# Performance work log

Hardware: AMD Instinct MI355X
Metric: run time of the kernel (lower is better)

The kernel has to match this reference:

```python
import jax, jax.numpy as jnp
import numpy as np

NUM_IN, NUM_OUT, SD, BATCH = 2048, 8192, 5, 4096
INIT_DELTA = 0.01


def _dist(a, b):
    # a: [I,1,D], b: [1,O,D] -> [I,O]
    return jnp.sqrt(jnp.sum((a - b) ** 2, axis=-1))


def setup_inputs() -> dict:
    key = jax.random.key(0)
    k1, k2, k3, k4, k5 = jax.random.split(key, 5)
    init_in_pos = jax.random.normal(k1, (NUM_IN, 1, SD), dtype=jnp.float32)
    init_out_pos = jax.random.normal(k2, (1, NUM_OUT, SD), dtype=jnp.float32)
    in_pos = init_in_pos + INIT_DELTA * jax.random.normal(k3, (NUM_IN, 1, SD), dtype=jnp.float32)
    out_pos = init_out_pos + INIT_DELTA * jax.random.normal(k4, (1, NUM_OUT, SD), dtype=jnp.float32)
    inputs = jax.random.normal(k5, (BATCH, NUM_IN), dtype=jnp.float32)
    biases = jnp.zeros((NUM_OUT,), dtype=jnp.float32)
    return {"inputs": inputs, "init_in_pos": init_in_pos, "init_out_pos": init_out_pos,
            "in_pos": in_pos, "out_pos": out_pos, "biases": biases}


def reference(inputs, init_in_pos, init_out_pos, in_pos, out_pos, biases):
    # weight = ||in_pos - out_pos|| - ||init_in_pos - init_out_pos||, shape [I,O]
    w = _dist(in_pos, out_pos) - _dist(init_in_pos, init_out_pos)
    return inputs @ w + biases
```

## Files before the change

kernel.cpp:

```cpp
#include <hip/hip_runtime.h>
#include <hip/hip_bf16.h>
#include <stdint.h>

#define NUM_IN  2048
#define NUM_OUT 8192
#define BATCH   4096
#define SD      5

#define BM 256
#define BN 256
#define BK 64
#define NT (NUM_IN / BK)
#define NI (NT / 2)
#define TILEE (BM * BK)

typedef __bf16 bf16x8 __attribute__((ext_vector_type(8)));
typedef float  f32x4  __attribute__((ext_vector_type(4)));
typedef unsigned short ushort_t;
typedef ushort_t ushort8 __attribute__((ext_vector_type(8)));

static __device__ __forceinline__ ushort_t bf16_bits(float f) {
  __hip_bfloat16 h = __float2bfloat16(f);
  ushort_t u;
  __builtin_memcpy(&u, &h, 2);
  return u;
}

__global__ __launch_bounds__(256) void cvt_kernel(const float* __restrict__ x,
                                                  ushort_t* __restrict__ y) {
  const int i = (blockIdx.x * 256 + threadIdx.x) * 8;
  float4 v0 = *reinterpret_cast<const float4*>(x + i);
  float4 v1 = *reinterpret_cast<const float4*>(x + i + 4);
  ushort8 o;
  o[0] = bf16_bits(v0.x); o[1] = bf16_bits(v0.y);
  o[2] = bf16_bits(v0.z); o[3] = bf16_bits(v0.w);
  o[4] = bf16_bits(v1.x); o[5] = bf16_bits(v1.y);
  o[6] = bf16_bits(v1.z); o[7] = bf16_bits(v1.w);
  *reinterpret_cast<ushort8*>(y + i) = o;
}

__global__ __launch_bounds__(256) void genw_kernel(
    const float* __restrict__ in_pos, const float* __restrict__ out_pos,
    const float* __restrict__ init_in, const float* __restrict__ init_out,
    ushort_t* __restrict__ Wt) {
  __shared__ float s_ip[NUM_IN * SD];
  __shared__ float s_iip[NUM_IN * SD];
  const int tid = threadIdx.x;
#pragma unroll
  for (int i = 0; i < 10; ++i) {
    const int idx = i * 1024 + tid * 4;
    *reinterpret_cast<float4*>(&s_ip[idx]) =
        *reinterpret_cast<const float4*>(in_pos + idx);
    *reinterpret_cast<float4*>(&s_iip[idx]) =
        *reinterpret_cast<const float4*>(init_in + idx);
  }
  __syncthreads();

  const int n  = blockIdx.x * 16 + (tid >> 4);
  const int kg = tid & 15;
  float op[SD], iop[SD];
#pragma unroll
  for (int d = 0; d < SD; ++d) {
    op[d]  = out_pos[n * SD + d];
    iop[d] = init_out[n * SD + d];
  }
#pragma unroll 1
  for (int kb = 0; kb < 16; ++kb) {
    const int k0 = kb * 128 + kg * 8;
    float buf[40], ibuf[40];
#pragma unroll
    for (int j = 0; j < 10; ++j) {
      float4 v = *reinterpret_cast<const float4*>(&s_ip[k0 * SD + j * 4]);
      buf[4 * j + 0] = v.x; buf[4 * j + 1] = v.y;
      buf[4 * j + 2] = v.z; buf[4 * j + 3] = v.w;
      float4 u = *reinterpret_cast<const float4*>(&s_iip[k0 * SD + j * 4]);
      ibuf[4 * j + 0] = u.x; ibuf[4 * j + 1] = u.y;
      ibuf[4 * j + 2] = u.z; ibuf[4 * j + 3] = u.w;
    }
    ushort8 o;
#pragma unroll
    for (int i = 0; i < 8; ++i) {
      float d1 = 0.f, d0 = 0.f;
#pragma unroll
      for (int d = 0; d < SD; ++d) {
        float a = buf[i * SD + d] - op[d];
        float b = ibuf[i * SD + d] - iop[d];
        d1 += a * a;
        d0 += b * b;
      }
      o[i] = bf16_bits(sqrtf(d1) - sqrtf(d0));
    }
    *reinterpret_cast<ushort8*>(Wt + (size_t)n * NUM_IN + k0) = o;
  }
}

__global__ __launch_bounds__(512, 1) void gemm_kernel(
    const ushort_t* __restrict__ A,
    const ushort_t* __restrict__ Bt,
    const float* __restrict__ bias,
    float* __restrict__ C) {
  __shared__ __align__(16) ushort_t sA[2 * TILEE];
  __shared__ __align__(16) ushort_t sB[2 * TILEE];

  const int tid  = threadIdx.x;
  const int w    = tid >> 6;
  const int l    = tid & 63;
  const int wm   = w >> 2;
  const int wn   = w & 3;
  const int lrow = l & 15;
  const int lkc  = l >> 4;

  const int orig = blockIdx.x;
  const int lin  = (orig & 7) * 64 + (orig >> 3);
  const int bx   = lin >> 4;
  const int by   = lin & 15;
  const int m0   = by * BM;
  const int n0   = bx * BN;

  const int ck0 = (lkc ^ (lrow & 7)) * 8;
  const int ck1 = ((4 + lkc) ^ (lrow & 7)) * 8;
  const int Ab  = wm * 4096 + lrow * 64;
  const int Bb  = wn * 2048 + lrow * 64;

  const int d0 = tid, d1 = tid + 512;
  const int lr0 = d0 >> 3, lr1 = d1 >> 3;
  const int c0 = (d0 & 7) ^ (lr0 & 7);
  const int c1 = (d1 & 7) ^ (lr1 & 7);
  const ushort_t* pA0 = A  + (size_t)(m0 + (lr0 >> 6) * 128 + (lr0 & 63)) * NUM_IN + c0 * 8;
  const ushort_t* pA1 = A  + (size_t)(m0 + (lr1 >> 6) * 128 + (lr1 & 63)) * NUM_IN + c1 * 8;
  const ushort_t* pB0 = Bt + (size_t)(n0 + (lr0 >> 5) * 64 + (lr0 & 31)) * NUM_IN + c0 * 8;
  const ushort_t* pB1 = Bt + (size_t)(n0 + (lr1 >> 5) * 64 + (lr1 & 31)) * NUM_IN + c1 * 8;

#define GLDS(src, dst)                                                         \
  __builtin_amdgcn_global_load_lds(                                            \
      reinterpret_cast<const __attribute__((address_space(1))) uint32_t*>(     \
          (uintptr_t)(src)),                                                   \
      reinterpret_cast<__attribute__((address_space(3))) uint32_t*>(           \
          (uintptr_t)(dst)),                                                   \
      16, 0, 0)

#define STAGE_A(bs, mh, kt)                                                    \
  {                                                                            \
    GLDS(pA0 + (size_t)(mh) * 64 * NUM_IN + (kt),                              \
         &sA[(bs) * TILEE + (mh) * 8192 + tid * 8]);                           \
    GLDS(pA1 + (size_t)(mh) * 64 * NUM_IN + (kt),                              \
         &sA[(bs) * TILEE + (mh) * 8192 + tid * 8 + 4096]);                    \
  }
#define STAGE_B(bs, nh, kt)                                                    \
  {                                                                            \
    GLDS(pB0 + (size_t)(nh) * 32 * NUM_IN + (kt),                              \
         &sB[(bs) * TILEE + (nh) * 8192 + tid * 8]);                           \
    GLDS(pB1 + (size_t)(nh) * 32 * NUM_IN + (kt),                              \
         &sB[(bs) * TILEE + (nh) * 8192 + tid * 8 + 4096]);                    \
  }

#define RD_A(bs, mh)                                                           \
  {                                                                            \
    _Pragma("unroll")                                                          \
    for (int mi = 0; mi < 4; ++mi) {                                           \
      a[mi][0] = *reinterpret_cast<const bf16x8*>(                             \
          &sA[(bs) * TILEE + (mh) * 8192 + Ab + mi * 1024 + ck0]);             \
      a[mi][1] = *reinterpret_cast<const bf16x8*>(                             \
          &sA[(bs) * TILEE + (mh) * 8192 + Ab + mi * 1024 + ck1]);             \
    }                                                                          \
  }
#define RD_B(bs, nh, arr)                                                      \
  {                                                                            \
    _Pragma("unroll")                                                          \
    for (int nj = 0; nj < 2; ++nj) {                                           \
      arr[nj][0] = *reinterpret_cast<const bf16x8*>(                           \
          &sB[(bs) * TILEE + (nh) * 8192 + Bb + nj * 1024 + ck0]);             \
      arr[nj][1] = *reinterpret_cast<const bf16x8*>(                           \
          &sB[(bs) * TILEE + (nh) * 8192 + Bb + nj * 1024 + ck1]);             \
    }                                                                          \
  }

#define MFMA_Q(mh, nh, arr)                                                    \
  {                                                                            \
    __builtin_amdgcn_s_setprio(1);                                             \
    _Pragma("unroll")                                                          \
    for (int mi = 0; mi < 4; ++mi)                                             \
      _Pragma("unroll")                                                        \
      for (int nj = 0; nj < 2; ++nj) {                                         \
        acc[(mh) * 4 + mi][(nh) * 2 + nj] =                                    \
            __builtin_amdgcn_mfma_f32_16x16x32_bf16(                           \
                a[mi][0], arr[nj][0], acc[(mh) * 4 + mi][(nh) * 2 + nj],       \
                0, 0, 0);                                                      \
        acc[(mh) * 4 + mi][(nh) * 2 + nj] =                                    \
            __builtin_amdgcn_mfma_f32_16x16x32_bf16(                           \
                a[mi][1], arr[nj][1], acc[(mh) * 4 + mi][(nh) * 2 + nj],       \
                0, 0, 0);                                                      \
      }                                                                        \
    __builtin_amdgcn_s_setprio(0);                                             \
  }

#define BARRIER  __builtin_amdgcn_s_barrier()
#define SCHED0   __builtin_amdgcn_sched_barrier(0)
#define LGKM0    asm volatile("s_waitcnt lgkmcnt(0)" ::: "memory")
#define VMCNT4   asm volatile("s_waitcnt vmcnt(4)" ::: "memory")

  f32x4 acc[8][4];
#pragma unroll
  for (int i = 0; i < 8; ++i)
#pragma unroll
    for (int j = 0; j < 4; ++j) acc[i][j] = f32x4{0.f, 0.f, 0.f, 0.f};

  STAGE_A(0, 0, 0) STAGE_B(0, 0, 0) STAGE_A(0, 1, 0) STAGE_B(0, 1, 0)
  STAGE_A(1, 0, BK) STAGE_B(1, 0, BK)
  VMCNT4;
  BARRIER;
  SCHED0;

#pragma unroll 1
  for (int it = 0; it < NI; ++it) {
    const int t1k = (2 * it + 1) * BK;
    const int t2  = 2 * it + 2, t3 = 2 * it + 3;
    const int t2k = (t2 < NT ? t2 : NT - 1) * BK;
    const int t3k = (t3 < NT ? t3 : NT - 1) * BK;
    bf16x8 a[4][2], b0[2][2], b1[2][2];

    RD_A(0, 0) RD_B(0, 0, b0)
    STAGE_A(1, 1, t1k)
    BARRIER; LGKM0; SCHED0;
    MFMA_Q(0, 0, b0)
    BARRIER; SCHED0;

    RD_B(0, 1, b1)
    STAGE_B(1, 1, t1k)
    BARRIER; LGKM0; SCHED0;
    MFMA_Q(0, 1, b1)
    BARRIER; SCHED0;

    RD_A(0, 1)
    STAGE_A(0, 0, t2k)
    BARRIER; LGKM0; SCHED0;
    MFMA_Q(1, 0, b0)
    BARRIER; SCHED0;

    STAGE_B(0, 0, t2k)
    BARRIER; SCHED0;
    MFMA_Q(1, 1, b1)
    VMCNT4;
    BARRIER; SCHED0;

    RD_A(1, 0) RD_B(1, 0, b0)
    STAGE_A(0, 1, t2k)
    BARRIER; LGKM0; SCHED0;
    MFMA_Q(0, 0, b0)
    BARRIER; SCHED0;

    RD_B(1, 1, b1)
    STAGE_B(0, 1, t2k)
    BARRIER; LGKM0; SCHED0;
    MFMA_Q(0, 1, b1)
    BARRIER; SCHED0;

    RD_A(1, 1)
    STAGE_A(1, 0, t3k)
    BARRIER; LGKM0; SCHED0;
    MFMA_Q(1, 0, b0)
    BARRIER; SCHED0;

    STAGE_B(1, 0, t3k)
    BARRIER; SCHED0;
    MFMA_Q(1, 1, b1)
    VMCNT4;
    BARRIER; SCHED0;
  }

  const int er = l >> 4;
  const int ec = l & 15;
#pragma unroll
  for (int nh = 0; nh < 2; ++nh) {
#pragma unroll
    for (int nj = 0; nj < 2; ++nj) {
      const int col = n0 + wn * 64 + nh * 32 + nj * 16 + ec;
      const float bi = bias[col];
#pragma unroll
      for (int mh = 0; mh < 2; ++mh) {
#pragma unroll
        for (int mi = 0; mi < 4; ++mi) {
#pragma unroll
          for (int j = 0; j < 4; ++j) {
            const int row = m0 + wm * 128 + mh * 64 + mi * 16 + er * 4 + j;
            C[(size_t)row * NUM_OUT + col] =
                acc[mh * 4 + mi][nh * 2 + nj][j] + bi;
          }
        }
      }
    }
  }
#undef STAGE_A
#undef STAGE_B
#undef RD_A
#undef RD_B
#undef MFMA_Q
#undef GLDS
}

extern "C" void kernel_launch(void* const* d_in, const int* in_sizes, int n_in,
                              void* d_out, int out_size, void* d_ws, size_t ws_size,
                              hipStream_t stream) {
  const float* inputs   = (const float*)d_in[0];
  const float* init_in  = (const float*)d_in[1];
  const float* init_out = (const float*)d_in[2];
  const float* in_pos   = (const float*)d_in[3];
  const float* out_pos  = (const float*)d_in[4];
  const float* biases   = (const float*)d_in[5];
  float* out = (float*)d_out;

  ushort_t* Abf = (ushort_t*)d_ws;
  ushort_t* Wt  = (ushort_t*)((char*)d_ws + (size_t)BATCH * NUM_IN * 2);

  cvt_kernel<<<(BATCH * NUM_IN) / (256 * 8), 256, 0, stream>>>(inputs, Abf);
  genw_kernel<<<NUM_OUT / 16, 256, 0, stream>>>(
      in_pos, out_pos, init_in, init_out, Wt);
  gemm_kernel<<<(BATCH / BM) * (NUM_OUT / BN), 512, 0, stream>>>(
      Abf, Wt, biases, out);
}
```

Baseline: 165.8 us.

## Deepen GEMM prefetch by one half-tile and drop scheduling barriers

Reorders the global-to-LDS staging so one more B half-tile is prefetched ahead (prologue stages seven halves, wait relaxed to vmcnt(6)), and shifts each stage one slot earlier in the eight-phase loop. It also removes all sched_barrier(0) fences, letting the compiler interleave instructions across phases. The intent is more latency hiding for global loads. The risks are LDS buffer overwrite hazards if the slot reuse ordering is wrong, and the compiler may schedule the MFMA/ds_read sequence worse without the fences.

Result: no change. 166.5 us (+0.4%).

```diff
diff --git a/kernel.cpp b/kernel.cpp
--- a/kernel.cpp
+++ b/kernel.cpp
@@ -195,9 +195,8 @@
   }
 
 #define BARRIER  __builtin_amdgcn_s_barrier()
-#define SCHED0   __builtin_amdgcn_sched_barrier(0)
 #define LGKM0    asm volatile("s_waitcnt lgkmcnt(0)" ::: "memory")
-#define VMCNT4   asm volatile("s_waitcnt vmcnt(4)" ::: "memory")
+#define VMCNT6   asm volatile("s_waitcnt vmcnt(6)" ::: "memory")
 
   f32x4 acc[8][4];
 #pragma unroll
@@ -205,67 +204,66 @@
 #pragma unroll
     for (int j = 0; j < 4; ++j) acc[i][j] = f32x4{0.f, 0.f, 0.f, 0.f};
 
-  STAGE_A(0, 0, 0) STAGE_B(0, 0, 0) STAGE_A(0, 1, 0) STAGE_B(0, 1, 0)
-  STAGE_A(1, 0, BK) STAGE_B(1, 0, BK)
-  VMCNT4;
+  STAGE_A(0, 0, 0) STAGE_B(0, 0, 0) STAGE_B(0, 1, 0) STAGE_A(0, 1, 0)
+  STAGE_A(1, 0, BK) STAGE_B(1, 0, BK) STAGE_B(1, 1, BK)
+  VMCNT6;
   BARRIER;
-  SCHED0;
 
 #pragma unroll 1
   for (int it = 0; it < NI; ++it) {
-    const int t1k = (2 * it + 1) * BK;
-    const int t2  = 2 * it + 2, t3 = 2 * it + 3;
-    const int t2k = (t2 < NT ? t2 : NT - 1) * BK;
-    const int t3k = (t3 < NT ? t3 : NT - 1) * BK;
+    const int ok  = (2 * it + 1) * BK;
+    const int e2  = 2 * it + 2, o2 = 2 * it + 3;
+    const int e2k = (e2 < NT ? e2 : NT - 1) * BK;
+    const int o2k = (o2 < NT ? o2 : NT - 1) * BK;
     bf16x8 a[4][2], b0[2][2], b1[2][2];
 
     RD_A(0, 0) RD_B(0, 0, b0)
-    STAGE_A(1, 1, t1k)
-    BARRIER; LGKM0; SCHED0;
+    STAGE_A(1, 1, ok)
+    BARRIER; LGKM0;
     MFMA_Q(0, 0, b0)
-    BARRIER; SCHED0;
+    BARRIER;
 
     RD_B(0, 1, b1)
-    STAGE_B(1, 1, t1k)
-    BARRIER; LGKM0; SCHED0;
+    STAGE_A(0, 0, e2k)
+    BARRIER; LGKM0;
     MFMA_Q(0, 1, b1)
-    BARRIER; SCHED0;
+    BARRIER;
 
     RD_A(0, 1)
-    STAGE_A(0, 0, t2k)
-    BARRIER; LGKM0; SCHED0;
+    STAGE_B(0, 0, e2k)
+    BARRIER; LGKM0;
     MFMA_Q(1, 0, b0)
-    BARRIER; SCHED0;
-
-    STAGE_B(0, 0, t2k)
-    BARRIER; SCHED0;
+    BARRIER;
+
+    STAGE_B(0, 1, e2k)
+    BARRIER;
     MFMA_Q(1, 1, b1)
-    VMCNT4;
-    BARRIER; SCHED0;
+    VMCNT6;
+    BARRIER;
 
     RD_A(1, 0) RD_B(1, 0, b0)
-    STAGE_A(0, 1, t2k)
-    BARRIER; LGKM0; SCHED0;
+    STAGE_A(0, 1, e2k)
+    BARRIER; LGKM0;
     MFMA_Q(0, 0, b0)
-    BARRIER; SCHED0;
+    BARRIER;
 
     RD_B(1, 1, b1)
-    STAGE_B(0, 1, t2k)
-    BARRIER; LGKM0; SCHED0;
+    STAGE_A(1, 0, o2k)
+    BARRIER; LGKM0;
     MFMA_Q(0, 1, b1)
-    BARRIER; SCHED0;
+    BARRIER;
 
     RD_A(1, 1)
-    STAGE_A(1, 0, t3k)
-    BARRIER; LGKM0; SCHED0;
+    STAGE_B(1, 0, o2k)
+    BARRIER; LGKM0;
     MFMA_Q(1, 0, b0)
-    BARRIER; SCHED0;
-
-    STAGE_B(1, 0, t3k)
-    BARRIER; SCHED0;
+    BARRIER;
+
+    STAGE_B(1, 1, o2k)
+    BARRIER;
     MFMA_Q(1, 1, b1)
-    VMCNT4;
-    BARRIER; SCHED0;
+    VMCNT6;
+    BARRIER;
   }
 
   const int er = l >> 4;
```

## Restructure GEMM main loop into per-k-tile schedule with fewer barriers

Applied to the files above, without the earlier changes.

Replaces the eight-phase ping-pong main loop, which had a workgroup barrier around every MFMA quarter, with a per-k-tile macro. The macro splits each tile's K into two halves and interleaves LDS reads, global-to-LDS staging of the next tile and MFMAs, using partial lgkmcnt waits and a single vmcnt(0) plus barrier per tile. The goal is to cut barrier stalls and overlap LDS reads with matrix math. In exchange, prefetch depth drops from about 1.5 tiles to one tile, and waiting on vmcnt(0) every tile may expose global load latency.

Measured after the change: 159.4 us. -3.9%, faster.

```diff
diff --git a/kernel.cpp b/kernel.cpp
--- a/kernel.cpp
+++ b/kernel.cpp
@@ -11,7 +11,6 @@
 #define BN 256
 #define BK 64
 #define NT (NUM_IN / BK)
-#define NI (NT / 2)
 #define TILEE (BM * BK)
 
 typedef __bf16 bf16x8 __attribute__((ext_vector_type(8)));
@@ -154,50 +153,68 @@
          &sB[(bs) * TILEE + (nh) * 8192 + tid * 8 + 4096]);                    \
   }
 
-#define RD_A(bs, mh)                                                           \
+#define RD_A(arr, bs, mh, ck)                                                  \
   {                                                                            \
     _Pragma("unroll")                                                          \
-    for (int mi = 0; mi < 4; ++mi) {                                           \
-      a[mi][0] = *reinterpret_cast<const bf16x8*>(                             \
-          &sA[(bs) * TILEE + (mh) * 8192 + Ab + mi * 1024 + ck0]);             \
-      a[mi][1] = *reinterpret_cast<const bf16x8*>(                             \
-          &sA[(bs) * TILEE + (mh) * 8192 + Ab + mi * 1024 + ck1]);             \
-    }                                                                          \
-  }
-#define RD_B(bs, nh, arr)                                                      \
+    for (int mi = 0; mi < 4; ++mi)                                             \
+      arr[mi] = *reinterpret_cast<const bf16x8*>(                              \
+          &sA[(bs) * TILEE + (mh) * 8192 + Ab + mi * 1024 + (ck)]);            \
+  }
+#define RD_B(arr, bs, nh, ck)                                                  \
   {                                                                            \
     _Pragma("unroll")                                                          \
-    for (int nj = 0; nj < 2; ++nj) {                                           \
-      arr[nj][0] = *reinterpret_cast<const bf16x8*>(                           \
-          &sB[(bs) * TILEE + (nh) * 8192 + Bb + nj * 1024 + ck0]);             \
-      arr[nj][1] = *reinterpret_cast<const bf16x8*>(                           \
-          &sB[(bs) * TILEE + (nh) * 8192 + Bb + nj * 1024 + ck1]);             \
-    }                                                                          \
-  }
-
-#define MFMA_Q(mh, nh, arr)                                                    \
+    for (int nj = 0; nj < 2; ++nj)                                             \
+      arr[nj] = *reinterpret_cast<const bf16x8*>(                              \
+          &sB[(bs) * TILEE + (nh) * 8192 + Bb + nj * 1024 + (ck)]);            \
+  }
+
+#define MFMA8(mh, nh, Aa, Bb_)                                                 \
   {                                                                            \
     __builtin_amdgcn_s_setprio(1);                                             \
     _Pragma("unroll")                                                          \
     for (int mi = 0; mi < 4; ++mi)                                             \
       _Pragma("unroll")                                                        \
-      for (int nj = 0; nj < 2; ++nj) {                                         \
+      for (int nj = 0; nj < 2; ++nj)                                           \
         acc[(mh) * 4 + mi][(nh) * 2 + nj] =                                    \
             __builtin_amdgcn_mfma_f32_16x16x32_bf16(                           \
-                a[mi][0], arr[nj][0], acc[(mh) * 4 + mi][(nh) * 2 + nj],       \
-                0, 0, 0);                                                      \
-        acc[(mh) * 4 + mi][(nh) * 2 + nj] =                                    \
-            __builtin_amdgcn_mfma_f32_16x16x32_bf16(                           \
-                a[mi][1], arr[nj][1], acc[(mh) * 4 + mi][(nh) * 2 + nj],       \
-                0, 0, 0);                                                      \
-      }                                                                        \
+                Aa[mi], Bb_[nj], acc[(mh) * 4 + mi][(nh) * 2 + nj], 0, 0, 0);  \
     __builtin_amdgcn_s_setprio(0);                                             \
   }
 
+#define LGKM(n)  asm volatile("s_waitcnt lgkmcnt(" #n ")" ::: "memory")
+#define SCHED0   __builtin_amdgcn_sched_barrier(0)
 #define BARRIER  __builtin_amdgcn_s_barrier()
-#define SCHED0   __builtin_amdgcn_sched_barrier(0)
-#define LGKM0    asm volatile("s_waitcnt lgkmcnt(0)" ::: "memory")
-#define VMCNT4   asm volatile("s_waitcnt vmcnt(4)" ::: "memory")
+#define VMCNT0   asm volatile("s_waitcnt vmcnt(0)" ::: "memory")
+
+#define KTILE(CUR, NXT, ktn)                                                   \
+  {                                                                            \
+    STAGE_A(NXT, 0, ktn)                                                       \
+    RD_A(aE, CUR, 0, ck0) RD_B(b0, CUR, 0, ck0)                                \
+    RD_B(b1, CUR, 1, ck0)                                    \
+    LGKM(2); SCHED0;                                                           \
+    MFMA8(0, 0, aE, b0)                                                        \
+    STAGE_B(NXT, 0, ktn)                                                       \
+    RD_A(aO, CUR, 1, ck0)                                    \
+    LGKM(4); SCHED0;                                                           \
+    MFMA8(0, 1, aE, b1)                                                        \
+    STAGE_A(NXT, 1, ktn)                                                       \
+    LGKM(0); SCHED0;                                                           \
+    MFMA8(1, 0, aO, b0)                                                        \
+    STAGE_B(NXT, 1, ktn)                                                       \
+    RD_A(aE, CUR, 0, ck1) RD_B(b0, CUR, 0, ck1)              \
+    MFMA8(1, 1, aO, b1)                                                        \
+    RD_B(b1, CUR, 1, ck1)                                    \
+    LGKM(2); SCHED0;                                                           \
+    MFMA8(0, 0, aE, b0)                                                        \
+    RD_A(aO, CUR, 1, ck1)                                    \
+    LGKM(4); SCHED0;                                                           \
+    MFMA8(0, 1, aE, b1)                                                        \
+    LGKM(0); SCHED0;                                                           \
+    MFMA8(1, 0, aO, b0)                                                        \
+    MFMA8(1, 1, aO, b1)                                                        \
+    VMCNT0;                                                                    \
+    BARRIER;                                                                   \
+  }
 
   f32x4 acc[8][4];
 #pragma unroll
@@ -205,67 +222,18 @@
 #pragma unroll
     for (int j = 0; j < 4; ++j) acc[i][j] = f32x4{0.f, 0.f, 0.f, 0.f};
 
+  bf16x8 aE[4], aO[4], b0[2], b1[2];
+
   STAGE_A(0, 0, 0) STAGE_B(0, 0, 0) STAGE_A(0, 1, 0) STAGE_B(0, 1, 0)
-  STAGE_A(1, 0, BK) STAGE_B(1, 0, BK)
-  VMCNT4;
+  VMCNT0;
   BARRIER;
-  SCHED0;
 
 #pragma unroll 1
-  for (int it = 0; it < NI; ++it) {
-    const int t1k = (2 * it + 1) * BK;
-    const int t2  = 2 * it + 2, t3 = 2 * it + 3;
-    const int t2k = (t2 < NT ? t2 : NT - 1) * BK;
-    const int t3k = (t3 < NT ? t3 : NT - 1) * BK;
-    bf16x8 a[4][2], b0[2][2], b1[2][2];
-
-    RD_A(0, 0) RD_B(0, 0, b0)
-    STAGE_A(1, 1, t1k)
-    BARRIER; LGKM0; SCHED0;
-    MFMA_Q(0, 0, b0)
-    BARRIER; SCHED0;
-
-    RD_B(0, 1, b1)
-    STAGE_B(1, 1, t1k)
-    BARRIER; LGKM0; SCHED0;
-    MFMA_Q(0, 1, b1)
-    BARRIER; SCHED0;
-
-    RD_A(0, 1)
-    STAGE_A(0, 0, t2k)
-    BARRIER; LGKM0; SCHED0;
-    MFMA_Q(1, 0, b0)
-    BARRIER; SCHED0;
-
-    STAGE_B(0, 0, t2k)
-    BARRIER; SCHED0;
-    MFMA_Q(1, 1, b1)
-    VMCNT4;
-    BARRIER; SCHED0;
-
-    RD_A(1, 0) RD_B(1, 0, b0)
-    STAGE_A(0, 1, t2k)
-    BARRIER; LGKM0; SCHED0;
-    MFMA_Q(0, 0, b0)
-    BARRIER; SCHED0;
-
-    RD_B(1, 1, b1)
-    STAGE_B(0, 1, t2k)
-    BARRIER; LGKM0; SCHED0;
-    MFMA_Q(0, 1, b1)
-    BARRIER; SCHED0;
-
-    RD_A(1, 1)
-    STAGE_A(1, 0, t3k)
-    BARRIER; LGKM0; SCHED0;
-    MFMA_Q(1, 0, b0)
-    BARRIER; SCHED0;
-
-    STAGE_B(1, 0, t3k)
-    BARRIER; SCHED0;
-    MFMA_Q(1, 1, b1)
-    VMCNT4;
-    BARRIER; SCHED0;
+  for (int tt = 0; tt < NT; tt += 2) {
+    const int k1 = (tt + 1) * BK;
+    const int k2 = (tt + 2 < NT ? tt + 2 : NT - 1) * BK;
+    KTILE(0, 1, k1)
+    KTILE(1, 0, k2)
   }
 
   const int er = l >> 4;
@@ -290,11 +258,12 @@
       }
     }
   }
+#undef KTILE
 #undef STAGE_A
 #undef STAGE_B
 #undef RD_A
 #undef RD_B
-#undef MFMA_Q
+#undef MFMA8
 #undef GLDS
 }
 
```
